# Kernel tuning notes

Measured on AMD Instinct MI355X. Metric: run time of the kernel, lower is better.

## Reference

```python
import jax, jax.numpy as jnp
import numpy as np

BS, NR, NC, EMB = 8, 2000, 2000, 128

def setup_inputs() -> dict:
    key = jax.random.key(0)
    k1, k2, k3, k4 = jax.random.split(key, 4)
    row_emb = jax.random.normal(k1, (BS, NR, EMB), dtype=jnp.float32)
    col_emb = jax.random.normal(k2, (BS, NC, EMB), dtype=jnp.float32)
    cost_mat = jax.random.uniform(k3, (BS, NR, NC), dtype=jnp.float32)
    # Linear(2*emb -> 1, bias=False): single weight vector of length 2*emb
    W = jax.random.normal(k4, (2 * EMB,), dtype=jnp.float32) * (1.0 / np.sqrt(2 * EMB))
    return {"row_emb": row_emb, "col_emb": col_emb, "cost_mat": cost_mat, "W": W}

def reference(row_emb, col_emb, cost_mat, W):
    emb = row_emb.shape[-1]
    w_row, w_col = W[:emb], W[emb:]
    # Decompose Linear on concat([row, col]) into two small projections
    row_proj = jnp.einsum('bre,e->br', row_emb, w_row)            # [B,R]
    col_proj = jnp.einsum('bce,e->bc', col_emb, w_col)            # [B,C]
    attn_logits = (row_proj[:, :, None] + col_proj[:, None, :]) * cost_mat  # [B,R,C]
    attn_act = jax.nn.leaky_relu(attn_logits, negative_slope=0.01)
    # self logit: Linear on concat([row, row]) = row @ (w_row + w_col)
    self_logit = jnp.einsum('bre,e->br', row_emb, w_row + w_col)  # [B,R]
    self_act = jax.nn.leaky_relu(self_logit, negative_slope=0.01)
    all_logits = jnp.concatenate([self_act[:, :, None], attn_act], axis=2)  # [B,R,1+C]
    scores = jax.nn.softmax(all_logits, axis=2)
    # weighted sum over values = [row_emb(self), col_emb...] without materializing [B,R,1+C,E]
    out = scores[:, :, 0:1] * row_emb + jnp.einsum('brc,bce->bre', scores[:, :, 1:], col_emb)
    return out  # [B,R,E]
```

## Files before the change

kernel.cpp:

```cpp
#include <hip/hip_runtime.h>
#include <hip/hip_bf16.h>
#include <cstdint>

#define BS  8
#define NR  2000
#define NC  2000
#define EMB 128

#define TRB   64
#define NTILE 32
#define NCHB  32

typedef float  f32x4  __attribute__((ext_vector_type(4)));
typedef __bf16 bf16x8 __attribute__((ext_vector_type(8)));

#define MFMA(a,b,c) __builtin_amdgcn_mfma_f32_16x16x32_bf16((a),(b),(c),0,0,0)

__global__ __launch_bounds__(256) void proj_kernel(
    const float* __restrict__ row_emb, const float* __restrict__ col_emb,
    const float* __restrict__ W,
    float* __restrict__ rp, float* __restrict__ cp, float* __restrict__ sa)
{
    int tid  = threadIdx.x;
    int lane = tid & 31;
    int sub  = tid >> 5;
    long long idx = (long long)blockIdx.x * 8 + sub;

    f32x4 wr = *(const f32x4*)(W + lane * 4);
    f32x4 wc = *(const f32x4*)(W + 128 + lane * 4);

    bool is_row = idx < (long long)BS * NR;
    const float* base = is_row ? (row_emb + idx * EMB)
                               : (col_emb + (idx - (long long)BS * NR) * EMB);
    f32x4 v = *(const f32x4*)(base + lane * 4);

    float d1, d2;
    if (is_row) {
        d1 = v.x * wr.x + v.y * wr.y + v.z * wr.z + v.w * wr.w;
        d2 = v.x * wc.x + v.y * wc.y + v.z * wc.z + v.w * wc.w;
    } else {
        d1 = v.x * wc.x + v.y * wc.y + v.z * wc.z + v.w * wc.w;
        d2 = 0.f;
    }
    #pragma unroll
    for (int m = 1; m < 32; m <<= 1) {
        d1 += __shfl_xor(d1, m);
        d2 += __shfl_xor(d2, m);
    }
    if (lane == 0) {
        if (is_row) {
            rp[idx] = d1;
            float s = d1 + d2;
            sa[idx] = fmaxf(s, 0.01f * s);
        } else {
            cp[idx - (long long)BS * NR] = d1;
        }
    }
}

__global__ __launch_bounds__(256) void maxcp_kernel(const float* __restrict__ cp,
                                                    float* __restrict__ maxcp)
{
    int b = blockIdx.x, tid = threadIdx.x;
    float m = -1e30f;
    for (int c = tid; c < NC; c += 256) m = fmaxf(m, cp[(size_t)b * NC + c]);
    #pragma unroll
    for (int s = 1; s < 64; s <<= 1) m = fmaxf(m, __shfl_xor(m, s));
    __shared__ float sm[4];
    if ((tid & 63) == 0) sm[tid >> 6] = m;
    __syncthreads();
    if (tid == 0)
        maxcp[b] = fmaxf(fmaxf(sm[0], sm[1]), fmaxf(sm[2], sm[3]));
}

__global__ __launch_bounds__(256) void colsplit_kernel(
    const float* __restrict__ col_emb, __bf16* __restrict__ colT)
{
    __shared__ float tile[64][EMB + 4];
    int tid = threadIdx.x;
    int b   = blockIdx.x >> 5;
    int kc  = blockIdx.x & 31;
    int c0  = kc * 64;

    #pragma unroll
    for (int i = 0; i < 8; ++i) {
        int flat = i * 256 + tid;
        int c = flat >> 5, e4 = (flat & 31) * 4;
        int cg = c0 + c;
        f32x4 v = {0.f, 0.f, 0.f, 0.f};
        if (cg < NC) v = *(const f32x4*)(col_emb + ((size_t)b * NC + cg) * EMB + e4);
        *(f32x4*)&tile[c][e4] = v;
    }
    __syncthreads();
    #pragma unroll
    for (int i = 0; i < 8; ++i) {
        int flat = i * 256 + tid;
        int hl = flat >> 10, e = (flat >> 3) & 127, sp = flat & 7;
        int cbase = 8 * (sp ^ (e & 7));
        bf16x8 v8;
        #pragma unroll
        for (int j = 0; j < 8; ++j) {
            float v = tile[cbase + j][e];
            __bf16 h = (__bf16)v;
            v8[j] = hl ? (__bf16)(v - (float)h) : h;
        }
        *(bf16x8*)(colT + ((size_t)(b * 32 + kc) * 16384 + (size_t)flat * 8)) = v8;
    }
}

__device__ __forceinline__ void gload16(const void* g, void* l) {
    __builtin_amdgcn_global_load_lds(
        (const __attribute__((address_space(1))) unsigned int*)g,
        (__attribute__((address_space(3))) unsigned int*)l, 16, 0, 0);
}

__global__ __launch_bounds__(512, 2) void main_kernel(
    const float* __restrict__ row_emb, const float* __restrict__ cost,
    const float* __restrict__ rp, const float* __restrict__ cp,
    const float* __restrict__ sa, const float* __restrict__ maxcp,
    const __bf16* __restrict__ colT, float* __restrict__ out)
{
    __shared__ __align__(16) __bf16 bbuf[16384];
    __shared__ __align__(16) __bf16 pbuf[8192];
    __shared__ float cp_sm[2048];
    __shared__ float M_sm[64], rp_sm[64], ps_sm[64], l_sm[64];

    const int tid  = threadIdx.x;
    const int b    = blockIdx.x & 7;
    const int tile = blockIdx.x >> 3;
    const int r0   = tile * TRB;

    const int w = tid >> 6, lane = tid & 63;
    const int khq = w & 1, ng = (w >> 1) & 1, mtp = w >> 2;

    const int p_row = tid >> 3, p_c8 = tid & 7;
    const int rg1 = r0 + p_row;
    const int rc1 = rg1 < NR ? rg1 : NR - 1;
    const float* cost_row = cost + ((size_t)b * NR + rc1) * NC;
    const __bf16* colTb = colT + (size_t)b * (NCHB * 16384);

    if (tid < 64) {
        int rg = r0 + tid, rc = rg < NR ? rg : NR - 1;
        float rpv = rp[(size_t)b * NR + rc], sav = sa[(size_t)b * NR + rc];
        float M = fmaxf(fmaxf(0.f, rpv + maxcp[b]), sav);
        M_sm[tid] = M; rp_sm[tid] = rpv; ps_sm[tid] = __expf(sav - M);
    }
    {
        int src = tid * 4; if (src > NC - 4) src = NC - 4;
        *(f32x4*)&cp_sm[tid * 4] = *(const f32x4*)&cp[(size_t)b * NC + src];
    }

    f32x4 acc[2][4];
    #pragma unroll
    for (int i = 0; i < 2; ++i)
        #pragma unroll
        for (int j = 0; j < 4; ++j) acc[i][j] = (f32x4){0,0,0,0};
    float lp = 0.f;
    float rp_r, M_r;

    auto LC = [&](int kc, f32x4& A, f32x4& B) {
        int base = kc * 64 + p_c8 * 8;
        if (base > NC - 8) base = NC - 8;
        A = *(const f32x4*)(cost_row + base);
        B = *(const f32x4*)(cost_row + base + 4);
    };
    auto PH1 = [&](int kc, f32x4 cA, f32x4 cB) {
        int gc = kc * 64 + p_c8 * 8;
        f32x4 q0 = *(const f32x4*)&cp_sm[gc];
        f32x4 q1 = *(const f32x4*)&cp_sm[gc + 4];
        bf16x8 hh, ll;
        #pragma unroll
        for (int j = 0; j < 8; ++j) {
            float cj  = j < 4 ? cA[j] : cB[j - 4];
            float cpj = j < 4 ? q0[j] : q1[j - 4];
            float logit = (rp_r + cpj) * cj;
            float act   = fmaxf(logit, 0.01f * logit);
            float pv    = __expf(act - M_r);
            pv = (gc + j < NC) ? pv : 0.f;
            lp += pv;
            __bf16 hb = (__bf16)pv;
            hh[j] = hb;
            ll[j] = (__bf16)(pv - (float)hb);
        }
        int ws8 = (p_c8 ^ (p_row & 7)) * 8;
        *(bf16x8*)&pbuf[p_row * 64 + ws8] = hh;
        *(bf16x8*)&pbuf[4096 + p_row * 64 + ws8] = ll;
    };
    auto PH2 = [&]() {
        bf16x8 Ah[2], Al[2];
        #pragma unroll
        for (int mti = 0; mti < 2; ++mti) {
            int m = mtp * 32 + mti * 16 + (lane & 15);
            int rs = ((khq * 4 + (lane >> 4)) ^ (m & 7)) * 8;
            Ah[mti] = *(const bf16x8*)&pbuf[m * 64 + rs];
            Al[mti] = *(const bf16x8*)&pbuf[4096 + m * 64 + rs];
        }
        #pragma unroll
        for (int nf = 0; nf < 4; ++nf) {
            int n = ng * 64 + nf * 16 + (lane & 15);
            int bs = ((khq * 4 + (lane >> 4)) ^ (n & 7)) * 8;
            bf16x8 Bh = *(const bf16x8*)&bbuf[n * 64 + bs];
            bf16x8 Bl = *(const bf16x8*)&bbuf[8192 + n * 64 + bs];
            #pragma unroll
            for (int mti = 0; mti < 2; ++mti) {
                acc[mti][nf] = MFMA(Ah[mti], Bh, acc[mti][nf]);
                acc[mti][nf] = MFMA(Al[mti], Bh, acc[mti][nf]);
                acc[mti][nf] = MFMA(Ah[mti], Bl, acc[mti][nf]);
            }
        }
    };

    #pragma unroll
    for (int j = 0; j < 4; ++j)
        gload16(colTb + (size_t)(j * 512 + tid) * 8, bbuf + (j * 512 + tid) * 8);
    asm volatile("" ::: "memory");
    f32x4 c00, c01; LC(0, c00, c01);
    asm volatile("" ::: "memory");
    f32x4 cc0, cc1; LC(1, cc0, cc1);
    asm volatile("" ::: "memory");
    __syncthreads();

    rp_r = rp_sm[p_row];
    M_r  = M_sm[p_row];

    PH1(0, c00, c01);
    asm volatile("s_waitcnt lgkmcnt(0)" ::: "memory");
    __builtin_amdgcn_s_barrier();

    for (int k = 0; k < NCHB - 1; ++k) {
        PH2();
        asm volatile("s_waitcnt lgkmcnt(0)" ::: "memory");
        __builtin_amdgcn_s_barrier();

        const __bf16* srcB = colTb + (size_t)(k + 1) * 16384;
        #pragma unroll
        for (int j = 0; j < 4; ++j)
            gload16(srcB + (size_t)(j * 512 + tid) * 8, bbuf + (j * 512 + tid) * 8);
        asm volatile("" ::: "memory");
        int k2 = (k + 2 < NCHB) ? k + 2 : NCHB - 1;
        f32x4 t0, t1; LC(k2, t0, t1);
        asm volatile("" ::: "memory");

        PH1(k + 1, cc0, cc1);
        cc0 = t0; cc1 = t1;

        asm volatile("s_waitcnt vmcnt(2) lgkmcnt(0)" ::: "memory");
        __builtin_amdgcn_s_barrier();
    }
    PH2();

    lp += __shfl_xor(lp, 1);
    lp += __shfl_xor(lp, 2);
    lp += __shfl_xor(lp, 4);
    if ((tid & 7) == 0) l_sm[p_row] = lp;
    __syncthreads();

    float* red = (float*)bbuf;
    if (khq == 1) {
        #pragma unroll
        for (int mti = 0; mti < 2; ++mti)
            #pragma unroll
            for (int nf = 0; nf < 4; ++nf)
                *(f32x4*)&red[(((mtp * 2 + ng) * 2 + mti) * 4 + nf) * 256 + lane * 4]
                    = acc[mti][nf];
    }
    __syncthreads();
    if (khq == 0) {
        const float* rowb = row_emb + (size_t)b * NR * EMB;
        float*       outb = out     + (size_t)b * NR * EMB;
        #pragma unroll
        for (int mti = 0; mti < 2; ++mti) {
            #pragma unroll
            for (int nf = 0; nf < 4; ++nf) {
                f32x4 o = acc[mti][nf];
                f32x4 r2 = *(const f32x4*)&red[(((mtp * 2 + ng) * 2 + mti) * 4 + nf) * 256 + lane * 4];
                o += r2;
                int col = ng * 64 + nf * 16 + (lane & 15);
                #pragma unroll
                for (int i = 0; i < 4; ++i) {
                    int row = mtp * 32 + mti * 16 + (lane >> 4) * 4 + i;
                    int rg  = r0 + row;
                    if (rg < NR) {
                        float ps  = ps_sm[row];
                        float inv = 1.0f / (ps + l_sm[row]);
                        float rv  = rowb[(size_t)rg * EMB + col];
                        outb[(size_t)rg * EMB + col] = (o[i] + rv * ps) * inv;
                    }
                }
            }
        }
    }
}

extern "C" void kernel_launch(void* const* d_in, const int* in_sizes, int n_in,
                              void* d_out, int out_size, void* d_ws, size_t ws_size,
                              hipStream_t stream) {
    const float* row_emb = (const float*)d_in[0];
    const float* col_emb = (const float*)d_in[1];
    const float* cost    = (const float*)d_in[2];
    const float* W       = (const float*)d_in[3];
    float* out = (float*)d_out;
    float* ws  = (float*)d_ws;

    float* rp = ws;
    float* sa = ws + 16000;
    float* cp = ws + 32000;
    float* mc = ws + 48000;
    __bf16* colT = (__bf16*)(ws + 48064);

    proj_kernel<<<4000, 256, 0, stream>>>(row_emb, col_emb, W, rp, cp, sa);
    maxcp_kernel<<<BS, 256, 0, stream>>>(cp, mc);
    colsplit_kernel<<<BS * 32, 256, 0, stream>>>(col_emb, colT);
    main_kernel<<<BS * NTILE, 512, 0, stream>>>(row_emb, cost, rp, cp, sa, mc,
                                                colT, out);
}
```

Before: 252.0 us.

## Halve row tile to 32 and double block occupancy with MFMA priority

Shrinks the per-block row tile from 64 to 32, so the grid doubles to 63 tiles per batch and the launch bound asks for 4 blocks per CU instead of 2. Each thread now handles 4 cost columns instead of 8, accumulators shrink to one M-tile, and the softmax partial reduction gains an extra shuffle step. It also raises wave priority around the MFMA block. The aim is more parallelism and better latency hiding, at the cost of loading the full colT B-operand stream twice as often per row, which doubles L2/HBM traffic for that operand.

```diff
diff --git a/kernel.cpp b/kernel.cpp
--- a/kernel.cpp
+++ b/kernel.cpp
@@ -7,11 +7,12 @@
 #define NC  2000
 #define EMB 128
 
-#define TRB   64
-#define NTILE 32
+#define TRB   32
+#define NTILE 63
 #define NCHB  32
 
 typedef float  f32x4  __attribute__((ext_vector_type(4)));
+typedef __bf16 bf16x4 __attribute__((ext_vector_type(4)));
 typedef __bf16 bf16x8 __attribute__((ext_vector_type(8)));
 
 #define MFMA(a,b,c) __builtin_amdgcn_mfma_f32_16x16x32_bf16((a),(b),(c),0,0,0)
@@ -114,16 +115,16 @@
         (__attribute__((address_space(3))) unsigned int*)l, 16, 0, 0);
 }
 
-__global__ __launch_bounds__(512, 2) void main_kernel(
+__global__ __launch_bounds__(512, 4) void main_kernel(
     const float* __restrict__ row_emb, const float* __restrict__ cost,
     const float* __restrict__ rp, const float* __restrict__ cp,
     const float* __restrict__ sa, const float* __restrict__ maxcp,
     const __bf16* __restrict__ colT, float* __restrict__ out)
 {
     __shared__ __align__(16) __bf16 bbuf[16384];
-    __shared__ __align__(16) __bf16 pbuf[8192];
+    __shared__ __align__(16) __bf16 pbuf[4096];
     __shared__ float cp_sm[2048];
-    __shared__ float M_sm[64], rp_sm[64], ps_sm[64], l_sm[64];
+    __shared__ float M_sm[TRB], rp_sm[TRB], ps_sm[TRB], l_sm[TRB];
 
     const int tid  = threadIdx.x;
     const int b    = blockIdx.x & 7;
@@ -133,13 +134,13 @@
     const int w = tid >> 6, lane = tid & 63;
     const int khq = w & 1, ng = (w >> 1) & 1, mtp = w >> 2;
 
-    const int p_row = tid >> 3, p_c8 = tid & 7;
+    const int p_row = tid >> 4, p_c4 = tid & 15;
     const int rg1 = r0 + p_row;
     const int rc1 = rg1 < NR ? rg1 : NR - 1;
     const float* cost_row = cost + ((size_t)b * NR + rc1) * NC;
     const __bf16* colTb = colT + (size_t)b * (NCHB * 16384);
 
-    if (tid < 64) {
+    if (tid < TRB) {
         int rg = r0 + tid, rc = rg < NR ? rg : NR - 1;
         float rpv = rp[(size_t)b * NR + rc], sav = sa[(size_t)b * NR + rc];
         float M = fmaxf(fmaxf(0.f, rpv + maxcp[b]), sav);
@@ -150,30 +151,24 @@
         *(f32x4*)&cp_sm[tid * 4] = *(const f32x4*)&cp[(size_t)b * NC + src];
     }
 
-    f32x4 acc[2][4];
-    #pragma unroll
-    for (int i = 0; i < 2; ++i)
-        #pragma unroll
-        for (int j = 0; j < 4; ++j) acc[i][j] = (f32x4){0,0,0,0};
+    f32x4 acc[4];
+    #pragma unroll
+    for (int j = 0; j < 4; ++j) acc[j] = (f32x4){0,0,0,0};
     float lp = 0.f;
     float rp_r, M_r;
 
-    auto LC = [&](int kc, f32x4& A, f32x4& B) {
-        int base = kc * 64 + p_c8 * 8;
-        if (base > NC - 8) base = NC - 8;
+    auto LC = [&](int kc, f32x4& A) {
+        int base = kc * 64 + p_c4 * 4;
+        if (base > NC - 4) base = NC - 4;
         A = *(const f32x4*)(cost_row + base);
-        B = *(const f32x4*)(cost_row + base + 4);
     };
-    auto PH1 = [&](int kc, f32x4 cA, f32x4 cB) {
-        int gc = kc * 64 + p_c8 * 8;
-        f32x4 q0 = *(const f32x4*)&cp_sm[gc];
-        f32x4 q1 = *(const f32x4*)&cp_sm[gc + 4];
-        bf16x8 hh, ll;
-        #pragma unroll
-        for (int j = 0; j < 8; ++j) {
-            float cj  = j < 4 ? cA[j] : cB[j - 4];
-            float cpj = j < 4 ? q0[j] : q1[j - 4];
-            float logit = (rp_r + cpj) * cj;
+    auto PH1 = [&](int kc, f32x4 cv) {
+        int gc = kc * 64 + p_c4 * 4;
+        f32x4 cpq = *(const f32x4*)&cp_sm[gc];
+        bf16x4 hh, ll;
+        #pragma unroll
+        for (int j = 0; j < 4; ++j) {
+            float logit = (rp_r + cpq[j]) * cv[j];
             float act   = fmaxf(logit, 0.01f * logit);
             float pv    = __expf(act - M_r);
             pv = (gc + j < NC) ? pv : 0.f;
@@ -182,48 +177,43 @@
             hh[j] = hb;
             ll[j] = (__bf16)(pv - (float)hb);
         }
-        int ws8 = (p_c8 ^ (p_row & 7)) * 8;
-        *(bf16x8*)&pbuf[p_row * 64 + ws8] = hh;
-        *(bf16x8*)&pbuf[4096 + p_row * 64 + ws8] = ll;
+        int slot = ((p_c4 >> 1) ^ (p_row & 7)) * 8 + (p_c4 & 1) * 4;
+        *(bf16x4*)&pbuf[p_row * 64 + slot] = hh;
+        *(bf16x4*)&pbuf[2048 + p_row * 64 + slot] = ll;
     };
     auto PH2 = [&]() {
-        bf16x8 Ah[2], Al[2];
-        #pragma unroll
-        for (int mti = 0; mti < 2; ++mti) {
-            int m = mtp * 32 + mti * 16 + (lane & 15);
-            int rs = ((khq * 4 + (lane >> 4)) ^ (m & 7)) * 8;
-            Ah[mti] = *(const bf16x8*)&pbuf[m * 64 + rs];
-            Al[mti] = *(const bf16x8*)&pbuf[4096 + m * 64 + rs];
-        }
+        const int m = mtp * 16 + (lane & 15);
+        const int rs = ((khq * 4 + (lane >> 4)) ^ (m & 7)) * 8;
+        bf16x8 Ah = *(const bf16x8*)&pbuf[m * 64 + rs];
+        bf16x8 Al = *(const bf16x8*)&pbuf[2048 + m * 64 + rs];
+        __builtin_amdgcn_s_setprio(1);
         #pragma unroll
         for (int nf = 0; nf < 4; ++nf) {
             int n = ng * 64 + nf * 16 + (lane & 15);
             int bs = ((khq * 4 + (lane >> 4)) ^ (n & 7)) * 8;
             bf16x8 Bh = *(const bf16x8*)&bbuf[n * 64 + bs];
             bf16x8 Bl = *(const bf16x8*)&bbuf[8192 + n * 64 + bs];
-            #pragma unroll
-            for (int mti = 0; mti < 2; ++mti) {
-                acc[mti][nf] = MFMA(Ah[mti], Bh, acc[mti][nf]);
-                acc[mti][nf] = MFMA(Al[mti], Bh, acc[mti][nf]);
-                acc[mti][nf] = MFMA(Ah[mti], Bl, acc[mti][nf]);
-            }
-        }
+            acc[nf] = MFMA(Ah, Bh, acc[nf]);
+            acc[nf] = MFMA(Al, Bh, acc[nf]);
+            acc[nf] = MFMA(Ah, Bl, acc[nf]);
+        }
+        __builtin_amdgcn_s_setprio(0);
     };
 
     #pragma unroll
     for (int j = 0; j < 4; ++j)
         gload16(colTb + (size_t)(j * 512 + tid) * 8, bbuf + (j * 512 + tid) * 8);
     asm volatile("" ::: "memory");
-    f32x4 c00, c01; LC(0, c00, c01);
+    f32x4 c0; LC(0, c0);
     asm volatile("" ::: "memory");
-    f32x4 cc0, cc1; LC(1, cc0, cc1);
+    f32x4 cc; LC(1, cc);
     asm volatile("" ::: "memory");
     __syncthreads();
 
     rp_r = rp_sm[p_row];
     M_r  = M_sm[p_row];
 
-    PH1(0, c00, c01);
+    PH1(0, c0);
     asm volatile("s_waitcnt lgkmcnt(0)" ::: "memory");
     __builtin_amdgcn_s_barrier();
 
@@ -238,13 +228,13 @@
             gload16(srcB + (size_t)(j * 512 + tid) * 8, bbuf + (j * 512 + tid) * 8);
         asm volatile("" ::: "memory");
         int k2 = (k + 2 < NCHB) ? k + 2 : NCHB - 1;
-        f32x4 t0, t1; LC(k2, t0, t1);
+        f32x4 t; LC(k2, t);
         asm volatile("" ::: "memory");
 
-        PH1(k + 1, cc0, cc1);
-        cc0 = t0; cc1 = t1;
-
-        asm volatile("s_waitcnt vmcnt(2) lgkmcnt(0)" ::: "memory");
+        PH1(k + 1, cc);
+        cc = t;
+
+        asm volatile("s_waitcnt vmcnt(1) lgkmcnt(0)" ::: "memory");
         __builtin_amdgcn_s_barrier();
     }
     PH2();
@@ -252,40 +242,35 @@
     lp += __shfl_xor(lp, 1);
     lp += __shfl_xor(lp, 2);
     lp += __shfl_xor(lp, 4);
-    if ((tid & 7) == 0) l_sm[p_row] = lp;
+    lp += __shfl_xor(lp, 8);
+    if ((tid & 15) == 0) l_sm[p_row] = lp;
     __syncthreads();
 
     float* red = (float*)bbuf;
     if (khq == 1) {
         #pragma unroll
-        for (int mti = 0; mti < 2; ++mti)
-            #pragma unroll
-            for (int nf = 0; nf < 4; ++nf)
-                *(f32x4*)&red[(((mtp * 2 + ng) * 2 + mti) * 4 + nf) * 256 + lane * 4]
-                    = acc[mti][nf];
+        for (int nf = 0; nf < 4; ++nf)
+            *(f32x4*)&red[((mtp * 2 + ng) * 4 + nf) * 256 + lane * 4] = acc[nf];
     }
     __syncthreads();
     if (khq == 0) {
         const float* rowb = row_emb + (size_t)b * NR * EMB;
         float*       outb = out     + (size_t)b * NR * EMB;
         #pragma unroll
-        for (int mti = 0; mti < 2; ++mti) {
+        for (int nf = 0; nf < 4; ++nf) {
+            f32x4 o = acc[nf];
+            f32x4 r2 = *(const f32x4*)&red[((mtp * 2 + ng) * 4 + nf) * 256 + lane * 4];
+            o += r2;
+            int col = ng * 64 + nf * 16 + (lane & 15);
             #pragma unroll
-            for (int nf = 0; nf < 4; ++nf) {
-                f32x4 o = acc[mti][nf];
-                f32x4 r2 = *(const f32x4*)&red[(((mtp * 2 + ng) * 2 + mti) * 4 + nf) * 256 + lane * 4];
-                o += r2;
-                int col = ng * 64 + nf * 16 + (lane & 15);
-                #pragma unroll
-                for (int i = 0; i < 4; ++i) {
-                    int row = mtp * 32 + mti * 16 + (lane >> 4) * 4 + i;
-                    int rg  = r0 + row;
-                    if (rg < NR) {
-                        float ps  = ps_sm[row];
-                        float inv = 1.0f / (ps + l_sm[row]);
-                        float rv  = rowb[(size_t)rg * EMB + col];
-                        outb[(size_t)rg * EMB + col] = (o[i] + rv * ps) * inv;
-                    }
+            for (int i = 0; i < 4; ++i) {
+                int row = mtp * 16 + (lane >> 4) * 4 + i;
+                int rg  = r0 + row;
+                if (rg < NR) {
+                    float ps  = ps_sm[row];
+                    float inv = 1.0f / (ps + l_sm[row]);
+                    float rv  = rowb[(size_t)rg * EMB + col];
+                    outb[(size_t)rg * EMB + col] = (o[i] + rv * ps) * inv;
                 }
             }
         }
```

New measurement: 236.6 us. 1.07x faster.
